# Optimization experiments

Measured on AMD Instinct MI355X. Metric: run time of the kernel, lower is better.

Reference implementation:

```python
import jax, jax.numpy as jnp
import numpy as np

N, F, E, G, NNZ = 16000, 128, 256000, 512, 512000


def _hconv(xin, row, col, hw_passed, W, b, n_nodes, n_edges):
    """PyG HypergraphConv (use_attention=False), faithful to the repo's call.
    xin: [n_nodes, Fin]; row=hyper_edge[0] (graph-edge ids), col=hyper_edge[1] (hyperedge ids).
    hw_passed: [NNZ] -- the repo passes node_weight[hyper_edge[1]]; PyG then indexes it
    again by hyperedge_index[1], so the effective per-incidence weight is hw_passed[col].
    """
    xw = xin @ W                                   # lin(x), bias=False in PyG
    w = hw_passed[col]                             # [NNZ]
    D = jax.ops.segment_sum(w, row, num_segments=n_nodes)
    Dinv = jnp.where(D == 0, 0.0, 1.0 / jnp.where(D == 0, 1.0, D))
    Bdeg = jax.ops.segment_sum(jnp.ones(row.shape, xw.dtype), col, num_segments=n_edges)
    Binv = jnp.where(Bdeg == 0, 0.0, 1.0 / jnp.where(Bdeg == 0, 1.0, Bdeg))
    # node -> hyperedge: message = B[col] * xw[row], sum over col
    out_e = jax.ops.segment_sum(Binv[col][:, None] * xw[row], col, num_segments=n_edges)
    # hyperedge -> node: message = D[row] * out_e[col], sum over row
    out = jax.ops.segment_sum(Dinv[row][:, None] * out_e[col], row, num_segments=n_nodes)
    return out + b


def setup_inputs() -> dict:
    key = jax.random.key(0)
    ks = jax.random.split(key, 20)
    rn = lambda k, shape, s=0.05: jax.random.normal(k, shape, dtype=jnp.float32) * s
    return {
        "x": jax.random.normal(ks[0], (N, F), dtype=jnp.float32),
        "graph_emb": jax.random.normal(ks[1], (G, F), dtype=jnp.float32),
        "edge_index": jax.random.randint(ks[2], (2, E), 0, N),
        "edge_type": jax.random.randint(ks[3], (E,), 0, 8),
        "batch": jnp.sort(jax.random.randint(ks[4], (N,), 0, G)),
        "hyper_edge": jnp.concatenate([
            jax.random.randint(ks[5], (1, NNZ), 0, E),   # graph-edge ids
            jax.random.randint(ks[6], (1, NNZ), 0, N)],  # hyperedge ids
            axis=0),
        # HyperWeight.lin: 2F -> F -> 1
        "hw_w1": rn(ks[7], (2 * F, F)), "hw_b1": jnp.zeros((F,), jnp.float32),
        "hw_w2": rn(ks[8], (F, 1)), "hw_b2": jnp.zeros((1,), jnp.float32),
        # HypergraphConv 1: 2F -> 2F; 2: 2F -> F (lin bias=False, separate out bias)
        "c1_w": rn(ks[9], (2 * F, 2 * F)), "c1_b": jnp.zeros((2 * F,), jnp.float32),
        "c2_w": rn(ks[10], (2 * F, F)), "c2_b": jnp.zeros((F,), jnp.float32),
        # Generator.lin: 3F -> 4F -> F
        "g_w1": rn(ks[11], (3 * F, 4 * F)), "g_b1": jnp.zeros((4 * F,), jnp.float32),
        "g_w2": rn(ks[12], (4 * F, F)), "g_b2": jnp.zeros((F,), jnp.float32),
        # classifier: 2F -> F -> 1
        "cl_w1": rn(ks[13], (2 * F, F)), "cl_b1": jnp.zeros((F,), jnp.float32),
        "cl_w2": rn(ks[14], (F, 1)), "cl_b2": jnp.zeros((1,), jnp.float32),
        "attn": jnp.array([0.5, 0.5], jnp.float32),
    }


def reference(x, graph_emb, edge_index, edge_type, batch, hyper_edge,
              hw_w1, hw_b1, hw_w2, hw_b2, c1_w, c1_b, c2_w, c2_b,
              g_w1, g_b1, g_w2, g_b2, cl_w1, cl_b1, cl_w2, cl_b2, attn):
    col, row = edge_index[0], edge_index[1]
    xij0 = jnp.concatenate([x[col], x[row]], axis=-1)          # [E, 2F]
    gemb = graph_emb[batch[edge_index[0]]]                     # [E, F] (unbatch_gemb)
    proto = graph_emb[batch]                                   # [N, F]
    # HyperWeight: per-node scalar weight
    h = jax.nn.relu(jnp.concatenate([x, proto], axis=-1) @ hw_w1 + hw_b1)
    node_w = jax.nn.sigmoid(h @ hw_w2 + hw_b2)[:, 0]           # [N]
    hrow, hcol = hyper_edge[0], hyper_edge[1]
    hw_passed = node_w[hcol]                                   # [NNZ], as in repo
    er = jax.nn.sigmoid(_hconv(xij0, hrow, hcol, hw_passed, c1_w, c1_b, E, N))
    sij = jax.nn.sigmoid(_hconv(er, hrow, hcol, hw_passed, c2_w, c2_b, E, N))  # [E, F]
    # Generator.lin on [xij, gemb]
    xl = jax.nn.relu(jnp.concatenate([xij0, gemb], axis=-1) @ g_w1 + g_b1)
    xl = jax.nn.relu(xl @ g_w2 + g_b2)                         # [E, F]
    s = attn[0] * xl + attn[1] * sij
    s = jnp.concatenate([s, gemb], axis=-1)                    # [E, 2F]
    s = jax.nn.relu(s @ cl_w1 + cl_b1)
    sij_out = jax.nn.sigmoid(s @ cl_w2 + cl_b2)                # [E, 1] (eval mode)
    return sij_out
```

## Files before the change

### kernel.cpp

```cpp
#include <hip/hip_runtime.h>
#include <hip/hip_bf16.h>

#define NODES  16000
#define FDIM   128
#define EDGES  256000
#define NNZ_   512000

typedef __attribute__((ext_vector_type(8))) short bf16x8;
typedef __attribute__((ext_vector_type(4))) float f32x4;

__device__ __forceinline__ float sigmoidf_(float z) { return 1.f / (1.f + __expf(-z)); }
__device__ __forceinline__ float bflo(unsigned u) { return __uint_as_float(u << 16); }
__device__ __forceinline__ float bfhi(unsigned u) { return __uint_as_float(u & 0xffff0000u); }
__device__ __forceinline__ unsigned pack2(float lo, float hi) {
    __hip_bfloat162 h;
    h.x = __float2bfloat16(lo);
    h.y = __float2bfloat16(hi);
    return *(unsigned*)&h;
}

__global__ __launch_bounds__(128) void hyperweight_k(
    const float* __restrict__ x, const float* __restrict__ ge, const int* __restrict__ batch,
    const float* __restrict__ w1, const float* __restrict__ b1,
    const float* __restrict__ w2, const float* __restrict__ b2, float* __restrict__ node_w)
{
    __shared__ float a[8][256];
    __shared__ float red[128];
    const int t = threadIdx.x;
    const int nb = blockIdx.x * 8;
    for (int u = 0; u < 8; ++u) {
        int n = nb + u;
        a[u][t]       = x[(size_t)n * FDIM + t];
        a[u][128 + t] = ge[(size_t)batch[n] * FDIM + t];
    }
    __syncthreads();
    float acc[8] = {0,0,0,0,0,0,0,0};
    for (int k = 0; k < 256; ++k) {
        float wv = w1[k * 128 + t];
        #pragma unroll
        for (int u = 0; u < 8; ++u) acc[u] += a[u][k] * wv;
    }
    const float wv2 = w2[t];
    for (int u = 0; u < 8; ++u) {
        float h = fmaxf(acc[u] + b1[t], 0.f);
        red[t] = h * wv2;
        __syncthreads();
        for (int s2 = 64; s2 > 0; s2 >>= 1) {
            if (t < s2) red[t] += red[t + s2];
            __syncthreads();
        }
        if (t == 0) node_w[nb + u] = sigmoidf_(red[0] + b2[0]);
        __syncthreads();
    }
}

__global__ void incidence_pass(const int* __restrict__ he, const float* __restrict__ node_w,
                               float* __restrict__ D, int* __restrict__ Bcnt, int* __restrict__ rowCnt)
{
    int i = blockIdx.x * 256 + threadIdx.x;
    if (i >= NNZ_) return;
    int hr = he[i];
    int hc = he[NNZ_ + i];
    int hc2 = he[NNZ_ + hc];
    atomicAdd(&D[hr], node_w[hc2]);
    atomicAdd(&Bcnt[hc], 1);
    atomicAdd(&rowCnt[hr], 1);
}

__global__ void inv_k(float* __restrict__ D, const int* __restrict__ Bcnt, float* __restrict__ Binv) {
    int i = blockIdx.x * 256 + threadIdx.x;
    if (i < EDGES) {
        float d = D[i];
        D[i] = (d != 0.f) ? 1.f / d : 0.f;
    }
    if (i < NODES) {
        int c = Bcnt[i];
        Binv[i] = c ? 1.f / (float)c : 0.f;
    }
}

__global__ __launch_bounds__(1024) void reduce_chunks(const int* __restrict__ in, int* __restrict__ part, int n) {
    __shared__ int s[1024];
    int t = threadIdx.x, g = blockIdx.x * 1024 + t;
    s[t] = (g < n) ? in[g] : 0;
    __syncthreads();
    for (int d = 512; d > 0; d >>= 1) {
        if (t < d) s[t] += s[t + d];
        __syncthreads();
    }
    if (t == 0) part[blockIdx.x] = s[0];
}
__global__ __launch_bounds__(1024) void scan_sums(int* __restrict__ part, int nc) {
    __shared__ int s[1024];
    int t = threadIdx.x;
    int v = (t < nc) ? part[t] : 0;
    s[t] = v;
    __syncthreads();
    for (int d = 1; d < 1024; d <<= 1) {
        int tv = (t >= d) ? s[t - d] : 0;
        __syncthreads();
        s[t] += tv;
        __syncthreads();
    }
    if (t < nc) part[t] = s[t] - v;
}
__global__ __launch_bounds__(1024) void scan_chunks(const int* __restrict__ in, const int* __restrict__ part,
                                                    int* __restrict__ out, int n) {
    __shared__ int s[1024];
    int t = threadIdx.x, g = blockIdx.x * 1024 + t;
    int v = (g < n) ? in[g] : 0;
    s[t] = v;
    __syncthreads();
    for (int d = 1; d < 1024; d <<= 1) {
        int tv = (t >= d) ? s[t - d] : 0;
        __syncthreads();
        s[t] += tv;
        __syncthreads();
    }
    int excl = s[t] - v + part[blockIdx.x];
    if (g < n) out[g] = excl;
    if (g == n - 1) out[n] = excl + v;
}

__global__ void scatter_pass(const int* __restrict__ he, const int* __restrict__ colOff, const int* __restrict__ rowOff,
                             int* __restrict__ colCur, int* __restrict__ rowCur,
                             int* __restrict__ colList, int* __restrict__ rowList)
{
    int i = blockIdx.x * 256 + threadIdx.x;
    if (i >= NNZ_) return;
    int hr = he[i];
    int hc = he[NNZ_ + i];
    int p = colOff[hc] + atomicAdd(&colCur[hc], 1);
    colList[p] = hr;
    int q = rowOff[hr] + atomicAdd(&rowCur[hr], 1);
    rowList[q] = hc;
}

__global__ void conv_bf16(const float* __restrict__ in, __hip_bfloat16* __restrict__ out, int n) {
    int i = blockIdx.x * 256 + threadIdx.x;
    if (i < n) out[i] = __float2bfloat16(in[i]);
}
__global__ void transpose_bf16(const float* __restrict__ in, __hip_bfloat16* __restrict__ out, int K, int N) {
    int i = blockIdx.x * 256 + threadIdx.x;
    if (i >= K * N) return;
    int n = i / K, k = i - n * K;
    out[i] = __float2bfloat16(in[k * N + n]);
}

__global__ __launch_bounds__(128) void col_gather_x(
    const __hip_bfloat16* __restrict__ xb, const int* __restrict__ ei,
    const int* __restrict__ colOff, const int* __restrict__ colList, float* __restrict__ agg)
{
    int n = blockIdx.x;
    int t = threadIdx.x;
    int base = (t < 64) ? 0 : EDGES;
    int f = t & 63;
    const unsigned* x32 = (const unsigned*)xb;
    int s = colOff[n], e = colOff[n + 1];
    float vx = 0.f, vy = 0.f;
    int j = s;
    for (; j + 3 < e; j += 4) {
        int r0 = colList[j], r1 = colList[j + 1], r2 = colList[j + 2], r3 = colList[j + 3];
        unsigned q0 = x32[(size_t)ei[base + r0] * 64 + f];
        unsigned q1 = x32[(size_t)ei[base + r1] * 64 + f];
        unsigned q2 = x32[(size_t)ei[base + r2] * 64 + f];
        unsigned q3 = x32[(size_t)ei[base + r3] * 64 + f];
        vx += bflo(q0) + bflo(q1) + bflo(q2) + bflo(q3);
        vy += bfhi(q0) + bfhi(q1) + bfhi(q2) + bfhi(q3);
    }
    for (; j < e; ++j) {
        unsigned q0 = x32[(size_t)ei[base + colList[j]] * 64 + f];
        vx += bflo(q0); vy += bfhi(q0);
    }
    int ob = (t < 64) ? 0 : 128;
    float2 o = make_float2(vx, vy);
    *(float2*)(agg + (size_t)n * 256 + ob + 2 * f) = o;
}

__global__ __launch_bounds__(128) void er_k(
    const __hip_bfloat16* __restrict__ oe1, const int* __restrict__ rowOff,
    const int* __restrict__ rowList, const float* __restrict__ Dinv,
    const float* __restrict__ c1b, __hip_bfloat16* __restrict__ er)
{
    int r = blockIdx.x;
    int t = threadIdx.x;
    int s = rowOff[r], e = rowOff[r + 1];
    const unsigned* o32 = (const unsigned*)oe1;
    float vx = 0.f, vy = 0.f;
    int j = s;
    for (; j + 1 < e; j += 2) {
        unsigned q0 = o32[(size_t)rowList[j] * 128 + t];
        unsigned q1 = o32[(size_t)rowList[j + 1] * 128 + t];
        vx += bflo(q0) + bflo(q1);
        vy += bfhi(q0) + bfhi(q1);
    }
    if (j < e) {
        unsigned q0 = o32[(size_t)rowList[j] * 128 + t];
        vx += bflo(q0); vy += bfhi(q0);
    }
    float dv = Dinv[r];
    *(unsigned*)(er + (size_t)r * 256 + 2 * t) =
        pack2(sigmoidf_(dv * vx + c1b[2 * t]), sigmoidf_(dv * vy + c1b[2 * t + 1]));
}

__global__ __launch_bounds__(128) void col_agg_er(
    const __hip_bfloat16* __restrict__ er, const int* __restrict__ colOff,
    const int* __restrict__ colList, float* __restrict__ agg)
{
    int n = blockIdx.x;
    int t = threadIdx.x;
    const unsigned* e32 = (const unsigned*)er;
    int s = colOff[n], e = colOff[n + 1];
    float vx = 0.f, vy = 0.f;
    int j = s;
    for (; j + 3 < e; j += 4) {
        unsigned q0 = e32[(size_t)colList[j]     * 128 + t];
        unsigned q1 = e32[(size_t)colList[j + 1] * 128 + t];
        unsigned q2 = e32[(size_t)colList[j + 2] * 128 + t];
        unsigned q3 = e32[(size_t)colList[j + 3] * 128 + t];
        vx += bflo(q0) + bflo(q1) + bflo(q2) + bflo(q3);
        vy += bfhi(q0) + bfhi(q1) + bfhi(q2) + bfhi(q3);
    }
    for (; j < e; ++j) {
        unsigned q0 = e32[(size_t)colList[j] * 128 + t];
        vx += bflo(q0); vy += bfhi(q0);
    }
    float2 o = make_float2(vx, vy);
    *(float2*)(agg + (size_t)n * 256 + 2 * t) = o;
}

template<int K, int NN, bool OB16>
__global__ __launch_bounds__(256) void gemm_node(
    const float* __restrict__ A, const float* __restrict__ B,
    const float* __restrict__ rowscale, void* __restrict__ C)
{
    __shared__ float As[16][68];
    __shared__ float Bs[16][68];
    const int tid = threadIdx.x;
    const int m0 = blockIdx.x * 64, n0 = blockIdx.y * 64;
    const int la_k = tid & 15, la_m = tid >> 4;
    const int lb_n = tid & 63, lb_k = tid >> 6;
    const int tn = tid & 15, tm = tid >> 4;
    float acc[4][4] = {};
    for (int k0 = 0; k0 < K; k0 += 16) {
        #pragma unroll
        for (int r = 0; r < 4; ++r)
            As[la_k][la_m + 16 * r] = A[(size_t)(m0 + la_m + 16 * r) * K + k0 + la_k];
        #pragma unroll
        for (int r = 0; r < 4; ++r)
            Bs[lb_k + 4 * r][lb_n] = B[(size_t)(k0 + lb_k + 4 * r) * NN + n0 + lb_n];
        __syncthreads();
        #pragma unroll
        for (int kk = 0; kk < 16; ++kk) {
            float4 av = *(const float4*)&As[kk][tm * 4];
            float4 bv = *(const float4*)&Bs[kk][tn * 4];
            float am[4] = {av.x, av.y, av.z, av.w};
            float bn[4] = {bv.x, bv.y, bv.z, bv.w};
            #pragma unroll
            for (int i = 0; i < 4; ++i)
                #pragma unroll
                for (int j = 0; j < 4; ++j)
                    acc[i][j] += am[i] * bn[j];
        }
        __syncthreads();
    }
    #pragma unroll
    for (int i = 0; i < 4; ++i) {
        int m = m0 + tm * 4 + i;
        float rs = rowscale[m];
        if constexpr (OB16) {
            __hip_bfloat16* Cp = (__hip_bfloat16*)C + (size_t)m * NN + n0 + tn * 4;
            #pragma unroll
            for (int j = 0; j < 4; ++j) Cp[j] = __float2bfloat16(rs * acc[i][j]);
        } else {
            float4 o = make_float4(rs * acc[i][0], rs * acc[i][1], rs * acc[i][2], rs * acc[i][3]);
            *(float4*)((float*)C + (size_t)m * NN + n0 + tn * 4) = o;
        }
    }
}

template<int K, int LDB>
__global__ __launch_bounds__(256) void xw_mfma(
    const __hip_bfloat16* __restrict__ A, const __hip_bfloat16* __restrict__ Bt,
    __hip_bfloat16* __restrict__ dst)
{
    __shared__ __align__(16) __hip_bfloat16 As[64][40];
    __shared__ __align__(16) __hip_bfloat16 Bs[128][40];
    const int tid = threadIdx.x;
    const int m0 = blockIdx.x * 64, n0 = blockIdx.y * 128;
    const int wave = tid >> 6, lane = tid & 63;
    const int wr = wave >> 1, wc = wave & 1;
    const int srow = tid >> 2, kseg = (tid & 3) * 8;
    const int nr = tid >> 1, kb = (tid & 1) * 16;
    const int fr = lane & 15, krow = (lane >> 4) * 8, rq = lane >> 4;

    f32x4 acc[2][4] = {};
    for (int k0 = 0; k0 < K; k0 += 32) {
        *(uint4*)&As[srow][kseg] = *(const uint4*)(A + (size_t)(m0 + srow) * K + k0 + kseg);
        *(uint4*)&Bs[nr][kb]     = *(const uint4*)(Bt + (size_t)(n0 + nr) * LDB + k0 + kb);
        *(uint4*)&Bs[nr][kb + 8] = *(const uint4*)(Bt + (size_t)(n0 + nr) * LDB + k0 + kb + 8);
        __syncthreads();
        bf16x8 af[2], bf[4];
        #pragma unroll
        for (int i = 0; i < 2; ++i) af[i] = *(const bf16x8*)&As[wr * 32 + i * 16 + fr][krow];
        #pragma unroll
        for (int j = 0; j < 4; ++j) bf[j] = *(const bf16x8*)&Bs[wc * 64 + j * 16 + fr][krow];
        #pragma unroll
        for (int i = 0; i < 2; ++i)
            #pragma unroll
            for (int j = 0; j < 4; ++j)
                acc[i][j] = __builtin_amdgcn_mfma_f32_16x16x32_bf16(af[i], bf[j], acc[i][j], 0, 0, 0);
        __syncthreads();
    }
    #pragma unroll
    for (int i = 0; i < 2; ++i)
        #pragma unroll
        for (int j = 0; j < 4; ++j) {
            int col = n0 + wc * 64 + j * 16 + fr;
            #pragma unroll
            for (int r = 0; r < 4; ++r) {
                int row = m0 + wr * 32 + i * 16 + rq * 4 + r;
                dst[(size_t)row * 512 + col] = __float2bfloat16(acc[i][j][r]);
            }
        }
}

__global__ __launch_bounds__(256) void gen2_mfma(
    const __hip_bfloat16* __restrict__ xa, const __hip_bfloat16* __restrict__ xb2,
    const __hip_bfloat16* __restrict__ gc, const float* __restrict__ b1,
    const __hip_bfloat16* __restrict__ gw2t, const float* __restrict__ b2,
    const int* __restrict__ ei, const int* __restrict__ batch,
    __hip_bfloat16* __restrict__ xl2)
{
    __shared__ __align__(16) __hip_bfloat16 As[2][64][40];
    __shared__ __align__(16) __hip_bfloat16 Bs[2][128][40];
    const int tid = threadIdx.x;
    const int m0 = blockIdx.x * 64;
    const int wave = tid >> 6, lane = tid & 63;
    const int wr = wave >> 1, wc = wave & 1;
    const int srow = tid >> 2, kseg = (tid & 3) * 8;
    const int nr = tid >> 1, kb = (tid & 1) * 16;
    const int fr = lane & 15, krow = (lane >> 4) * 8, rq = lane >> 4;

    const int eg = m0 + srow;
    const int c = ei[eg];
    const __hip_bfloat16* pa = xa  + (size_t)c * 512;
    const __hip_bfloat16* pb = xb2 + (size_t)ei[EDGES + eg] * 512;
    const __hip_bfloat16* pc = gc  + (size_t)batch[c] * 512;

    uint4 ua, ub, uc, bv0, bv1;
    auto GLOAD = [&](int k0) {
        int kg = k0 + kseg;
        ua = *(const uint4*)(pa + kg);
        ub = *(const uint4*)(pb + kg);
        uc = *(const uint4*)(pc + kg);
        bv0 = *(const uint4*)(gw2t + (size_t)nr * 512 + k0 + kb);
        bv1 = *(const uint4*)(gw2t + (size_t)nr * 512 + k0 + kb + 8);
    };
    auto STORE = [&](int buf, int k0) {
        int kg = k0 + kseg;
        float4 f0 = *(const float4*)(b1 + kg);
        float4 f1 = *(const float4*)(b1 + kg + 4);
        uint4 av;
        av.x = pack2(fmaxf(bflo(ua.x) + bflo(ub.x) + bflo(uc.x) + f0.x, 0.f),
                     fmaxf(bfhi(ua.x) + bfhi(ub.x) + bfhi(uc.x) + f0.y, 0.f));
        av.y = pack2(fmaxf(bflo(ua.y) + bflo(ub.y) + bflo(uc.y) + f0.z, 0.f),
                     fmaxf(bfhi(ua.y) + bfhi(ub.y) + bfhi(uc.y) + f0.w, 0.f));
        av.z = pack2(fmaxf(bflo(ua.z) + bflo(ub.z) + bflo(uc.z) + f1.x, 0.f),
                     fmaxf(bfhi(ua.z) + bfhi(ub.z) + bfhi(uc.z) + f1.y, 0.f));
        av.w = pack2(fmaxf(bflo(ua.w) + bflo(ub.w) + bflo(uc.w) + f1.z, 0.f),
                     fmaxf(bfhi(ua.w) + bfhi(ub.w) + bfhi(uc.w) + f1.w, 0.f));
        *(uint4*)&As[buf][srow][kseg] = av;
        *(uint4*)&Bs[buf][nr][kb]     = bv0;
        *(uint4*)&Bs[buf][nr][kb + 8] = bv1;
    };

    GLOAD(0);
    STORE(0, 0);
    __syncthreads();

    f32x4 acc[2][4] = {};
    for (int it = 0; it < 16; ++it) {
        int cur = it & 1;
        if (it < 15) GLOAD((it + 1) * 32);
        bf16x8 af[2], bf[4];
        #pragma unroll
        for (int i = 0; i < 2; ++i) af[i] = *(const bf16x8*)&As[cur][wr * 32 + i * 16 + fr][krow];
        #pragma unroll
        for (int j = 0; j < 4; ++j) bf[j] = *(const bf16x8*)&Bs[cur][wc * 64 + j * 16 + fr][krow];
        #pragma unroll
        for (int i = 0; i < 2; ++i)
            #pragma unroll
            for (int j = 0; j < 4; ++j)
                acc[i][j] = __builtin_amdgcn_mfma_f32_16x16x32_bf16(af[i], bf[j], acc[i][j], 0, 0, 0);
        if (it < 15) STORE(cur ^ 1, (it + 1) * 32);
        __syncthreads();
    }
    #pragma unroll
    for (int i = 0; i < 2; ++i)
        #pragma unroll
        for (int j = 0; j < 4; ++j) {
            int col = wc * 64 + j * 16 + fr;
            float bc = b2[col];
            #pragma unroll
            for (int r = 0; r < 4; ++r) {
                int row = m0 + wr * 32 + i * 16 + rq * 4 + r;
                xl2[(size_t)row * 128 + col] = __float2bfloat16(fmaxf(acc[i][j][r] + bc, 0.f));
            }
        }
}

__global__ __launch_bounds__(256) void cls_mfma(
    const __hip_bfloat16* __restrict__ xl2, const __hip_bfloat16* __restrict__ oe2,
    const __hip_bfloat16* __restrict__ geb, const float* __restrict__ attn,
    const __hip_bfloat16* __restrict__ clw1t, const float* __restrict__ b1,
    const float* __restrict__ w2, const float* __restrict__ b2, const float* __restrict__ c2b,
    const int* __restrict__ ei, const int* __restrict__ batch,
    const int* __restrict__ rowOff, const int* __restrict__ rowList, const float* __restrict__ Dinv,
    float* __restrict__ out)
{
    __shared__ __align__(16) __hip_bfloat16 As[2][64][40];
    __shared__ __align__(16) __hip_bfloat16 Bs[2][128][40];
    const int tid = threadIdx.x;
    const int m0 = blockIdx.x * 64;
    const int wave = tid >> 6, lane = tid & 63;
    const int srow = tid >> 2, kseg = (tid & 3) * 8;
    const int nr = tid >> 1, kb = (tid & 1) * 16;
    const int fr = lane & 15, krow = (lane >> 4) * 8, rq = lane >> 4;

    const int eg = m0 + srow;
    const int gi = batch[ei[eg]];
    const float a0 = attn[0], a1 = attn[1];
    const int rs = rowOff[eg], re = rowOff[eg + 1];
    const float dv = Dinv[eg];

    uint4 avr, bv0, bv1;
    auto PREP = [&](int k0) {
        int kg = k0 + kseg;
        bv0 = *(const uint4*)(clw1t + (size_t)nr * 256 + k0 + kb);
        bv1 = *(const uint4*)(clw1t + (size_t)nr * 256 + k0 + kb + 8);
        if (kg < 128) {
            uint4 u = *(const uint4*)(xl2 + (size_t)eg * 128 + kg);
            float s0 = 0.f, s1 = 0.f, s2 = 0.f, s3 = 0.f, s4 = 0.f, s5 = 0.f, s6 = 0.f, s7 = 0.f;
            for (int q = rs; q < re; ++q) {
                uint4 o = *(const uint4*)(oe2 + (size_t)rowList[q] * 128 + kg);
                s0 += bflo(o.x); s1 += bfhi(o.x); s2 += bflo(o.y); s3 += bfhi(o.y);
                s4 += bflo(o.z); s5 += bfhi(o.z); s6 += bflo(o.w); s7 += bfhi(o.w);
            }
            float4 c0 = *(const float4*)(c2b + kg);
            float4 c1 = *(const float4*)(c2b + kg + 4);
            avr.x = pack2(a0 * bflo(u.x) + a1 * sigmoidf_(dv * s0 + c0.x),
                          a0 * bfhi(u.x) + a1 * sigmoidf_(dv * s1 + c0.y));
            avr.y = pack2(a0 * bflo(u.y) + a1 * sigmoidf_(dv * s2 + c0.z),
                          a0 * bfhi(u.y) + a1 * sigmoidf_(dv * s3 + c0.w));
            avr.z = pack2(a0 * bflo(u.z) + a1 * sigmoidf_(dv * s4 + c1.x),
                          a0 * bfhi(u.z) + a1 * sigmoidf_(dv * s5 + c1.y));
            avr.w = pack2(a0 * bflo(u.w) + a1 * sigmoidf_(dv * s6 + c1.z),
                          a0 * bfhi(u.w) + a1 * sigmoidf_(dv * s7 + c1.w));
        } else {
            avr = *(const uint4*)(geb + (size_t)gi * 128 + kg - 128);
        }
    };
    auto STORE = [&](int buf) {
        *(uint4*)&As[buf][srow][kseg] = avr;
        *(uint4*)&Bs[buf][nr][kb]     = bv0;
        *(uint4*)&Bs[buf][nr][kb + 8] = bv1;
    };

    PREP(0);
    STORE(0);
    __syncthreads();

    f32x4 acc[8] = {};
    for (int it = 0; it < 8; ++it) {
        int cur = it & 1;
        if (it < 7) PREP((it + 1) * 32);
        bf16x8 af = *(const bf16x8*)&As[cur][wave * 16 + fr][krow];
        #pragma unroll
        for (int j = 0; j < 8; ++j) {
            bf16x8 bf = *(const bf16x8*)&Bs[cur][j * 16 + fr][krow];
            acc[j] = __builtin_amdgcn_mfma_f32_16x16x32_bf16(af, bf, acc[j], 0, 0, 0);
        }
        if (it < 7) STORE(cur ^ 1);
        __syncthreads();
    }
    float rsum[4] = {0.f, 0.f, 0.f, 0.f};
    #pragma unroll
    for (int j = 0; j < 8; ++j) {
        int colg = j * 16 + fr;
        float bc = b1[colg];
        float wv = w2[colg];
        #pragma unroll
        for (int r = 0; r < 4; ++r)
            rsum[r] += fmaxf(acc[j][r] + bc, 0.f) * wv;
    }
    #pragma unroll
    for (int m = 1; m < 16; m <<= 1) {
        #pragma unroll
        for (int r = 0; r < 4; ++r) rsum[r] += __shfl_xor(rsum[r], m, 64);
    }
    if (fr == 0) {
        float bb = b2[0];
        #pragma unroll
        for (int r = 0; r < 4; ++r)
            out[m0 + wave * 16 + rq * 4 + r] = sigmoidf_(rsum[r] + bb);
    }
}

extern "C" void kernel_launch(void* const* d_in, const int* in_sizes, int n_in,
                              void* d_out, int out_size, void* d_ws, size_t ws_size,
                              hipStream_t stream)
{
    const float* x     = (const float*)d_in[0];
    const float* ge    = (const float*)d_in[1];
    const int*   ei    = (const int*)d_in[2];
    const int*   batch = (const int*)d_in[4];
    const int*   he    = (const int*)d_in[5];
    const float* hw_w1 = (const float*)d_in[6];
    const float* hw_b1 = (const float*)d_in[7];
    const float* hw_w2 = (const float*)d_in[8];
    const float* hw_b2 = (const float*)d_in[9];
    const float* c1_w  = (const float*)d_in[10];
    const float* c1_b  = (const float*)d_in[11];
    const float* c2_w  = (const float*)d_in[12];
    const float* c2_b  = (const float*)d_in[13];
    const float* g_w1  = (const float*)d_in[14];
    const float* g_b1  = (const float*)d_in[15];
    const float* g_w2  = (const float*)d_in[16];
    const float* g_b2  = (const float*)d_in[17];
    const float* cl_w1 = (const float*)d_in[18];
    const float* cl_b1 = (const float*)d_in[19];
    const float* cl_w2 = (const float*)d_in[20];
    const float* cl_b2 = (const float*)d_in[21];
    const float* attn  = (const float*)d_in[22];
    float* out = (float*)d_out;

    char* ws = (char*)d_ws;
    size_t off = 0;
    auto alloc = [&](size_t nb) -> void* {
        off = (off + 255) & ~(size_t)255;
        void* p = ws + off;
        off += nb;
        return p;
    };
    float* D      = (float*)alloc((size_t)EDGES * 4);
    int*   Bcnt   = (int*)  alloc((size_t)NODES * 4);
    int*   rowCnt = (int*)  alloc((size_t)EDGES * 4);
    int*   colCur = (int*)  alloc((size_t)NODES * 4);
    int*   rowCur = (int*)  alloc((size_t)EDGES * 4);
    size_t zero_end = off;
    float* node_w = (float*)alloc((size_t)NODES * 4);
    float* Binv   = (float*)alloc((size_t)NODES * 4);
    int*   colOff = (int*)  alloc((size_t)(NODES + 1) * 4);
    int*   rowOff = (int*)  alloc((size_t)(EDGES + 1) * 4);
    int*   colList= (int*)  alloc((size_t)NNZ_ * 4);
    int*   rowList= (int*)  alloc((size_t)NNZ_ * 4);
    int*   partA  = (int*)  alloc(1024 * 4);
    int*   partB  = (int*)  alloc(1024 * 4);
    __hip_bfloat16* xb    = (__hip_bfloat16*)alloc((size_t)NODES * FDIM * 2);
    __hip_bfloat16* geb   = (__hip_bfloat16*)alloc((size_t)512 * FDIM * 2);
    __hip_bfloat16* gw1t  = (__hip_bfloat16*)alloc((size_t)512 * 384 * 2);
    __hip_bfloat16* gw2t  = (__hip_bfloat16*)alloc((size_t)128 * 512 * 2);
    __hip_bfloat16* clw1t = (__hip_bfloat16*)alloc((size_t)128 * 256 * 2);
    __hip_bfloat16* xa    = (__hip_bfloat16*)alloc((size_t)NODES * 512 * 2);
    __hip_bfloat16* xb2   = (__hip_bfloat16*)alloc((size_t)NODES * 512 * 2);
    __hip_bfloat16* gc    = (__hip_bfloat16*)alloc((size_t)512 * 512 * 2);
    float* agg  = (float*)alloc((size_t)NODES * 256 * 4);
    __hip_bfloat16* oe1b = (__hip_bfloat16*)alloc((size_t)NODES * 256 * 2);
    __hip_bfloat16* oe2  = (__hip_bfloat16*)alloc((size_t)NODES * 128 * 2);
    __hip_bfloat16* er   = (__hip_bfloat16*)alloc((size_t)EDGES * 256 * 2);
    __hip_bfloat16* xl2  = er;

    hipMemsetAsync(D, 0, zero_end, stream);

    hyperweight_k<<<NODES / 8, 128, 0, stream>>>(x, ge, batch, hw_w1, hw_b1, hw_w2, hw_b2, node_w);
    incidence_pass<<<NNZ_ / 256, 256, 0, stream>>>(he, node_w, D, Bcnt, rowCnt);
    inv_k<<<EDGES / 256, 256, 0, stream>>>(D, Bcnt, Binv);

    const int ncN = (NODES + 1023) / 1024;
    const int ncE = (EDGES + 1023) / 1024;
    reduce_chunks<<<ncN, 1024, 0, stream>>>(Bcnt, partA, NODES);
    scan_sums<<<1, 1024, 0, stream>>>(partA, ncN);
    scan_chunks<<<ncN, 1024, 0, stream>>>(Bcnt, partA, colOff, NODES);
    reduce_chunks<<<ncE, 1024, 0, stream>>>(rowCnt, partB, EDGES);
    scan_sums<<<1, 1024, 0, stream>>>(partB, ncE);
    scan_chunks<<<ncE, 1024, 0, stream>>>(rowCnt, partB, rowOff, EDGES);
    scatter_pass<<<NNZ_ / 256, 256, 0, stream>>>(he, colOff, rowOff, colCur, rowCur, colList, rowList);

    conv_bf16<<<(NODES * FDIM + 255) / 256, 256, 0, stream>>>(x, xb, NODES * FDIM);
    conv_bf16<<<(512 * FDIM + 255) / 256, 256, 0, stream>>>(ge, geb, 512 * FDIM);
    transpose_bf16<<<(384 * 512 + 255) / 256, 256, 0, stream>>>(g_w1, gw1t, 384, 512);
    transpose_bf16<<<(512 * 128 + 255) / 256, 256, 0, stream>>>(g_w2, gw2t, 512, 128);
    transpose_bf16<<<(256 * 128 + 255) / 256, 256, 0, stream>>>(cl_w1, clw1t, 256, 128);

    xw_mfma<128, 384><<<dim3(NODES / 64, 4), 256, 0, stream>>>(xb, gw1t, xa);
    xw_mfma<128, 384><<<dim3(NODES / 64, 4), 256, 0, stream>>>(xb, gw1t + 128, xb2);
    xw_mfma<128, 384><<<dim3(512 / 64, 4), 256, 0, stream>>>(geb, gw1t + 256, gc);

    col_gather_x<<<NODES, 128, 0, stream>>>(xb, ei, colOff, colList, agg);
    gemm_node<256, 256, true><<<dim3(NODES / 64, 4), 256, 0, stream>>>(agg, c1_w, Binv, oe1b);

    er_k<<<EDGES, 128, 0, stream>>>(oe1b, rowOff, rowList, D, c1_b, er);
    col_agg_er<<<NODES, 128, 0, stream>>>(er, colOff, colList, agg);
    gemm_node<256, 128, true><<<dim3(NODES / 64, 2), 256, 0, stream>>>(agg, c2_w, Binv, oe2);

    gen2_mfma<<<EDGES / 64, 256, 0, stream>>>(xa, xb2, gc, g_b1, gw2t, g_b2, ei, batch, xl2);

    cls_mfma<<<EDGES / 64, 256, 0, stream>>>(xl2, oe2, geb, attn, clw1t, cl_b1, cl_w2, cl_b2,
                                             c2_b, ei, batch, rowOff, rowList, D, out);
}
```

Baseline: 770.5 us.

## Fuse generator and classifier edge GEMMs, fold graph term into xa, switch to fp16

Merges gen2_mfma and cls_mfma into one kernel that keeps the 64x128 generator output tile in shared memory, so the per-edge intermediate never goes through global memory. The graph-embedding projection and first bias are added into the per-node xa product at its epilogue, which removes one gather and add per edge in the hot loop. Edge-side operands move to fp16 so the add and relu can use packed v_pk_add/v_pk_max. In exchange the fused kernel drops the software double-buffering, uses more LDS per block, and fp16 has less range than bf16.

New measurement: 731.1 us. -5.1%, faster.

```diff
diff --git a/kernel.cpp b/kernel.cpp
--- a/kernel.cpp
+++ b/kernel.cpp
@@ -1,5 +1,6 @@
 #include <hip/hip_runtime.h>
 #include <hip/hip_bf16.h>
+#include <hip/hip_fp16.h>
 
 #define NODES  16000
 #define FDIM   128
@@ -7,6 +8,7 @@
 #define NNZ_   512000
 
 typedef __attribute__((ext_vector_type(8))) short bf16x8;
+typedef __attribute__((ext_vector_type(8))) _Float16 f16x8;
 typedef __attribute__((ext_vector_type(4))) float f32x4;
 
 __device__ __forceinline__ float sigmoidf_(float z) { return 1.f / (1.f + __expf(-z)); }
@@ -17,6 +19,19 @@
     h.x = __float2bfloat16(lo);
     h.y = __float2bfloat16(hi);
     return *(unsigned*)&h;
+}
+__device__ __forceinline__ unsigned pk_add_f16(unsigned a, unsigned b) {
+    unsigned r; asm("v_pk_add_f16 %0, %1, %2" : "=v"(r) : "v"(a), "v"(b)); return r;
+}
+__device__ __forceinline__ unsigned pk_relu_f16(unsigned a) {
+    unsigned r; asm("v_pk_max_f16 %0, %1, %2" : "=v"(r) : "v"(a), "v"(0u)); return r;
+}
+__device__ __forceinline__ unsigned pkh(float lo, float hi) {
+    __half2 h = __floats2half2_rn(lo, hi);
+    return *(unsigned*)&h;
+}
+__device__ __forceinline__ float2 h2f2(unsigned u) {
+    return __half22float2(*(__half2*)&u);
 }
 
 __global__ __launch_bounds__(128) void hyperweight_k(
@@ -136,15 +151,20 @@
     rowList[q] = hc;
 }
 
-__global__ void conv_bf16(const float* __restrict__ in, __hip_bfloat16* __restrict__ out, int n) {
+__global__ void conv_x(const float* __restrict__ in, __hip_bfloat16* __restrict__ ob,
+                       _Float16* __restrict__ oh, int n) {
     int i = blockIdx.x * 256 + threadIdx.x;
-    if (i < n) out[i] = __float2bfloat16(in[i]);
-}
-__global__ void transpose_bf16(const float* __restrict__ in, __hip_bfloat16* __restrict__ out, int K, int N) {
+    if (i < n) { float v = in[i]; ob[i] = __float2bfloat16(v); oh[i] = (_Float16)v; }
+}
+__global__ void conv_f16(const float* __restrict__ in, _Float16* __restrict__ out, int n) {
+    int i = blockIdx.x * 256 + threadIdx.x;
+    if (i < n) out[i] = (_Float16)in[i];
+}
+__global__ void transpose_f16(const float* __restrict__ in, _Float16* __restrict__ out, int K, int N) {
     int i = blockIdx.x * 256 + threadIdx.x;
     if (i >= K * N) return;
     int n = i / K, k = i - n * K;
-    out[i] = __float2bfloat16(in[k * N + n]);
+    out[i] = (_Float16)in[k * N + n];
 }
 
 __global__ __launch_bounds__(128) void col_gather_x(
@@ -279,13 +299,13 @@
     }
 }
 
-template<int K, int LDB>
-__global__ __launch_bounds__(256) void xw_mfma(
-    const __hip_bfloat16* __restrict__ A, const __hip_bfloat16* __restrict__ Bt,
-    __hip_bfloat16* __restrict__ dst)
-{
-    __shared__ __align__(16) __hip_bfloat16 As[64][40];
-    __shared__ __align__(16) __hip_bfloat16 Bs[128][40];
+template<int LDB, bool XAG>
+__global__ __launch_bounds__(256) void xw_f16(
+    const _Float16* __restrict__ A, const _Float16* __restrict__ Bt, _Float16* __restrict__ dst,
+    const _Float16* __restrict__ gct, const int* __restrict__ batch, const float* __restrict__ bias)
+{
+    __shared__ __align__(16) _Float16 As[64][40];
+    __shared__ __align__(16) _Float16 Bs[128][40];
     const int tid = threadIdx.x;
     const int m0 = blockIdx.x * 64, n0 = blockIdx.y * 128;
     const int wave = tid >> 6, lane = tid & 63;
@@ -295,21 +315,21 @@
     const int fr = lane & 15, krow = (lane >> 4) * 8, rq = lane >> 4;
 
     f32x4 acc[2][4] = {};
-    for (int k0 = 0; k0 < K; k0 += 32) {
-        *(uint4*)&As[srow][kseg] = *(const uint4*)(A + (size_t)(m0 + srow) * K + k0 + kseg);
+    for (int k0 = 0; k0 < 128; k0 += 32) {
+        *(uint4*)&As[srow][kseg] = *(const uint4*)(A + (size_t)(m0 + srow) * 128 + k0 + kseg);
         *(uint4*)&Bs[nr][kb]     = *(const uint4*)(Bt + (size_t)(n0 + nr) * LDB + k0 + kb);
         *(uint4*)&Bs[nr][kb + 8] = *(const uint4*)(Bt + (size_t)(n0 + nr) * LDB + k0 + kb + 8);
         __syncthreads();
-        bf16x8 af[2], bf[4];
-        #pragma unroll
-        for (int i = 0; i < 2; ++i) af[i] = *(const bf16x8*)&As[wr * 32 + i * 16 + fr][krow];
-        #pragma unroll
-        for (int j = 0; j < 4; ++j) bf[j] = *(const bf16x8*)&Bs[wc * 64 + j * 16 + fr][krow];
+        f16x8 af[2], bf[4];
+        #pragma unroll
+        for (int i = 0; i < 2; ++i) af[i] = *(const f16x8*)&As[wr * 32 + i * 16 + fr][krow];
+        #pragma unroll
+        for (int j = 0; j < 4; ++j) bf[j] = *(const f16x8*)&Bs[wc * 64 + j * 16 + fr][krow];
         #pragma unroll
         for (int i = 0; i < 2; ++i)
             #pragma unroll
             for (int j = 0; j < 4; ++j)
-                acc[i][j] = __builtin_amdgcn_mfma_f32_16x16x32_bf16(af[i], bf[j], acc[i][j], 0, 0, 0);
+                acc[i][j] = __builtin_amdgcn_mfma_f32_16x16x32_f16(af[i], bf[j], acc[i][j], 0, 0, 0);
         __syncthreads();
     }
     #pragma unroll
@@ -320,20 +340,28 @@
             #pragma unroll
             for (int r = 0; r < 4; ++r) {
                 int row = m0 + wr * 32 + i * 16 + rq * 4 + r;
-                dst[(size_t)row * 512 + col] = __float2bfloat16(acc[i][j][r]);
+                float v = acc[i][j][r];
+                if constexpr (XAG)
+                    v += (float)gct[(size_t)batch[row] * 512 + col] + bias[col];
+                dst[(size_t)row * 512 + col] = (_Float16)v;
             }
         }
 }
 
-__global__ __launch_bounds__(256) void gen2_mfma(
-    const __hip_bfloat16* __restrict__ xa, const __hip_bfloat16* __restrict__ xb2,
-    const __hip_bfloat16* __restrict__ gc, const float* __restrict__ b1,
-    const __hip_bfloat16* __restrict__ gw2t, const float* __restrict__ b2,
+__global__ __launch_bounds__(256) void gencls_mfma(
+    const _Float16* __restrict__ xag, const _Float16* __restrict__ xb2,
+    const _Float16* __restrict__ gw2t, const float* __restrict__ gb2,
+    const _Float16* __restrict__ geh, const float* __restrict__ attn,
+    const _Float16* __restrict__ clw1t, const float* __restrict__ clb1,
+    const float* __restrict__ w2, const float* __restrict__ b2, const float* __restrict__ c2b,
+    const __hip_bfloat16* __restrict__ oe2,
     const int* __restrict__ ei, const int* __restrict__ batch,
-    __hip_bfloat16* __restrict__ xl2)
-{
-    __shared__ __align__(16) __hip_bfloat16 As[2][64][40];
-    __shared__ __align__(16) __hip_bfloat16 Bs[2][128][40];
+    const int* __restrict__ rowOff, const int* __restrict__ rowList, const float* __restrict__ Dinv,
+    float* __restrict__ out)
+{
+    __shared__ __align__(16) _Float16 As[64][40];
+    __shared__ __align__(16) _Float16 Bs[128][40];
+    __shared__ __align__(16) _Float16 xlt[64][128];
     const int tid = threadIdx.x;
     const int m0 = blockIdx.x * 64;
     const int wave = tid >> 6, lane = tid & 63;
@@ -343,57 +371,37 @@
     const int fr = lane & 15, krow = (lane >> 4) * 8, rq = lane >> 4;
 
     const int eg = m0 + srow;
-    const int c = ei[eg];
-    const __hip_bfloat16* pa = xa  + (size_t)c * 512;
-    const __hip_bfloat16* pb = xb2 + (size_t)ei[EDGES + eg] * 512;
-    const __hip_bfloat16* pc = gc  + (size_t)batch[c] * 512;
-
-    uint4 ua, ub, uc, bv0, bv1;
-    auto GLOAD = [&](int k0) {
+    const int cnode = ei[eg];
+    const _Float16* pa = xag + (size_t)cnode * 512;
+    const _Float16* pb = xb2 + (size_t)ei[EDGES + eg] * 512;
+    const int gi = batch[cnode];
+    const int rs = rowOff[eg], re = rowOff[eg + 1];
+    const float dv = Dinv[eg];
+
+    f32x4 acc[2][4] = {};
+    for (int k0 = 0; k0 < 512; k0 += 32) {
         int kg = k0 + kseg;
-        ua = *(const uint4*)(pa + kg);
-        ub = *(const uint4*)(pb + kg);
-        uc = *(const uint4*)(pc + kg);
-        bv0 = *(const uint4*)(gw2t + (size_t)nr * 512 + k0 + kb);
-        bv1 = *(const uint4*)(gw2t + (size_t)nr * 512 + k0 + kb + 8);
-    };
-    auto STORE = [&](int buf, int k0) {
-        int kg = k0 + kseg;
-        float4 f0 = *(const float4*)(b1 + kg);
-        float4 f1 = *(const float4*)(b1 + kg + 4);
+        uint4 ua = *(const uint4*)(pa + kg);
+        uint4 ub = *(const uint4*)(pb + kg);
         uint4 av;
-        av.x = pack2(fmaxf(bflo(ua.x) + bflo(ub.x) + bflo(uc.x) + f0.x, 0.f),
-                     fmaxf(bfhi(ua.x) + bfhi(ub.x) + bfhi(uc.x) + f0.y, 0.f));
-        av.y = pack2(fmaxf(bflo(ua.y) + bflo(ub.y) + bflo(uc.y) + f0.z, 0.f),
-                     fmaxf(bfhi(ua.y) + bfhi(ub.y) + bfhi(uc.y) + f0.w, 0.f));
-        av.z = pack2(fmaxf(bflo(ua.z) + bflo(ub.z) + bflo(uc.z) + f1.x, 0.f),
-                     fmaxf(bfhi(ua.z) + bfhi(ub.z) + bfhi(uc.z) + f1.y, 0.f));
-        av.w = pack2(fmaxf(bflo(ua.w) + bflo(ub.w) + bflo(uc.w) + f1.z, 0.f),
-                     fmaxf(bfhi(ua.w) + bfhi(ub.w) + bfhi(uc.w) + f1.w, 0.f));
-        *(uint4*)&As[buf][srow][kseg] = av;
-        *(uint4*)&Bs[buf][nr][kb]     = bv0;
-        *(uint4*)&Bs[buf][nr][kb + 8] = bv1;
-    };
-
-    GLOAD(0);
-    STORE(0, 0);
-    __syncthreads();
-
-    f32x4 acc[2][4] = {};
-    for (int it = 0; it < 16; ++it) {
-        int cur = it & 1;
-        if (it < 15) GLOAD((it + 1) * 32);
-        bf16x8 af[2], bf[4];
-        #pragma unroll
-        for (int i = 0; i < 2; ++i) af[i] = *(const bf16x8*)&As[cur][wr * 32 + i * 16 + fr][krow];
-        #pragma unroll
-        for (int j = 0; j < 4; ++j) bf[j] = *(const bf16x8*)&Bs[cur][wc * 64 + j * 16 + fr][krow];
+        av.x = pk_relu_f16(pk_add_f16(ua.x, ub.x));
+        av.y = pk_relu_f16(pk_add_f16(ua.y, ub.y));
+        av.z = pk_relu_f16(pk_add_f16(ua.z, ub.z));
+        av.w = pk_relu_f16(pk_add_f16(ua.w, ub.w));
+        *(uint4*)&As[srow][kseg] = av;
+        *(uint4*)&Bs[nr][kb]     = *(const uint4*)(gw2t + (size_t)nr * 512 + k0 + kb);
+        *(uint4*)&Bs[nr][kb + 8] = *(const uint4*)(gw2t + (size_t)nr * 512 + k0 + kb + 8);
+        __syncthreads();
+        f16x8 af[2], bf[4];
+        #pragma unroll
+        for (int i = 0; i < 2; ++i) af[i] = *(const f16x8*)&As[wr * 32 + i * 16 + fr][krow];
+        #pragma unroll
+        for (int j = 0; j < 4; ++j) bf[j] = *(const f16x8*)&Bs[wc * 64 + j * 16 + fr][krow];
         #pragma unroll
         for (int i = 0; i < 2; ++i)
             #pragma unroll
             for (int j = 0; j < 4; ++j)
-                acc[i][j] = __builtin_amdgcn_mfma_f32_16x16x32_bf16(af[i], bf[j], acc[i][j], 0, 0, 0);
-        if (it < 15) STORE(cur ^ 1, (it + 1) * 32);
+                acc[i][j] = __builtin_amdgcn_mfma_f32_16x16x32_f16(af[i], bf[j], acc[i][j], 0, 0, 0);
         __syncthreads();
     }
     #pragma unroll
@@ -401,46 +409,22 @@
         #pragma unroll
         for (int j = 0; j < 4; ++j) {
             int col = wc * 64 + j * 16 + fr;
-            float bc = b2[col];
+            float bc = gb2[col];
             #pragma unroll
             for (int r = 0; r < 4; ++r) {
-                int row = m0 + wr * 32 + i * 16 + rq * 4 + r;
-                xl2[(size_t)row * 128 + col] = __float2bfloat16(fmaxf(acc[i][j][r] + bc, 0.f));
+                int row = wr * 32 + i * 16 + rq * 4 + r;
+                xlt[row][col] = (_Float16)fmaxf(acc[i][j][r] + bc, 0.f);
             }
         }
-}
-
-__global__ __launch_bounds__(256) void cls_mfma(
-    const __hip_bfloat16* __restrict__ xl2, const __hip_bfloat16* __restrict__ oe2,
-    const __hip_bfloat16* __restrict__ geb, const float* __restrict__ attn,
-    const __hip_bfloat16* __restrict__ clw1t, const float* __restrict__ b1,
-    const float* __restrict__ w2, const float* __restrict__ b2, const float* __restrict__ c2b,
-    const int* __restrict__ ei, const int* __restrict__ batch,
-    const int* __restrict__ rowOff, const int* __restrict__ rowList, const float* __restrict__ Dinv,
-    float* __restrict__ out)
-{
-    __shared__ __align__(16) __hip_bfloat16 As[2][64][40];
-    __shared__ __align__(16) __hip_bfloat16 Bs[2][128][40];
-    const int tid = threadIdx.x;
-    const int m0 = blockIdx.x * 64;
-    const int wave = tid >> 6, lane = tid & 63;
-    const int srow = tid >> 2, kseg = (tid & 3) * 8;
-    const int nr = tid >> 1, kb = (tid & 1) * 16;
-    const int fr = lane & 15, krow = (lane >> 4) * 8, rq = lane >> 4;
-
-    const int eg = m0 + srow;
-    const int gi = batch[ei[eg]];
+    __syncthreads();
+
     const float a0 = attn[0], a1 = attn[1];
-    const int rs = rowOff[eg], re = rowOff[eg + 1];
-    const float dv = Dinv[eg];
-
-    uint4 avr, bv0, bv1;
-    auto PREP = [&](int k0) {
-        int kg = k0 + kseg;
-        bv0 = *(const uint4*)(clw1t + (size_t)nr * 256 + k0 + kb);
-        bv1 = *(const uint4*)(clw1t + (size_t)nr * 256 + k0 + kb + 8);
+    f32x4 acc2[8] = {};
+    for (int it = 0; it < 8; ++it) {
+        int k0 = it * 32, kg = k0 + kseg;
+        uint4 av;
         if (kg < 128) {
-            uint4 u = *(const uint4*)(xl2 + (size_t)eg * 128 + kg);
+            uint4 u = *(const uint4*)&xlt[srow][kg];
             float s0 = 0.f, s1 = 0.f, s2 = 0.f, s3 = 0.f, s4 = 0.f, s5 = 0.f, s6 = 0.f, s7 = 0.f;
             for (int q = rs; q < re; ++q) {
                 uint4 o = *(const uint4*)(oe2 + (size_t)rowList[q] * 128 + kg);
@@ -449,50 +433,39 @@
             }
             float4 c0 = *(const float4*)(c2b + kg);
             float4 c1 = *(const float4*)(c2b + kg + 4);
-            avr.x = pack2(a0 * bflo(u.x) + a1 * sigmoidf_(dv * s0 + c0.x),
-                          a0 * bfhi(u.x) + a1 * sigmoidf_(dv * s1 + c0.y));
-            avr.y = pack2(a0 * bflo(u.y) + a1 * sigmoidf_(dv * s2 + c0.z),
-                          a0 * bfhi(u.y) + a1 * sigmoidf_(dv * s3 + c0.w));
-            avr.z = pack2(a0 * bflo(u.z) + a1 * sigmoidf_(dv * s4 + c1.x),
-                          a0 * bfhi(u.z) + a1 * sigmoidf_(dv * s5 + c1.y));
-            avr.w = pack2(a0 * bflo(u.w) + a1 * sigmoidf_(dv * s6 + c1.z),
-                          a0 * bfhi(u.w) + a1 * sigmoidf_(dv * s7 + c1.w));
+            float2 f0 = h2f2(u.x), f1 = h2f2(u.y), f2 = h2f2(u.z), f3 = h2f2(u.w);
+            av.x = pkh(a0 * f0.x + a1 * sigmoidf_(dv * s0 + c0.x),
+                       a0 * f0.y + a1 * sigmoidf_(dv * s1 + c0.y));
+            av.y = pkh(a0 * f1.x + a1 * sigmoidf_(dv * s2 + c0.z),
+                       a0 * f1.y + a1 * sigmoidf_(dv * s3 + c0.w));
+            av.z = pkh(a0 * f2.x + a1 * sigmoidf_(dv * s4 + c1.x),
+                       a0 * f2.y + a1 * sigmoidf_(dv * s5 + c1.y));
+            av.w = pkh(a0 * f3.x + a1 * sigmoidf_(dv * s6 + c1.z),
+                       a0 * f3.y + a1 * sigmoidf_(dv * s7 + c1.w));
         } else {
-            avr = *(const uint4*)(geb + (size_t)gi * 128 + kg - 128);
-        }
-    };
-    auto STORE = [&](int buf) {
-        *(uint4*)&As[buf][srow][kseg] = avr;
-        *(uint4*)&Bs[buf][nr][kb]     = bv0;
-        *(uint4*)&Bs[buf][nr][kb + 8] = bv1;
-    };
-
-    PREP(0);
-    STORE(0);
-    __syncthreads();
-
-    f32x4 acc[8] = {};
-    for (int it = 0; it < 8; ++it) {
-        int cur = it & 1;
-        if (it < 7) PREP((it + 1) * 32);
-        bf16x8 af = *(const bf16x8*)&As[cur][wave * 16 + fr][krow];
+            av = *(const uint4*)(geh + (size_t)gi * 128 + kg - 128);
+        }
+        *(uint4*)&As[srow][kseg] = av;
+        *(uint4*)&Bs[nr][kb]     = *(const uint4*)(clw1t + (size_t)nr * 256 + k0 + kb);
+        *(uint4*)&Bs[nr][kb + 8] = *(const uint4*)(clw1t + (size_t)nr * 256 + k0 + kb + 8);
+        __syncthreads();
+        f16x8 af = *(const f16x8*)&As[wave * 16 + fr][krow];
         #pragma unroll
         for (int j = 0; j < 8; ++j) {
-            bf16x8 bf = *(const bf16x8*)&Bs[cur][j * 16 + fr][krow];
-            acc[j] = __builtin_amdgcn_mfma_f32_16x16x32_bf16(af, bf, acc[j], 0, 0, 0);
-        }
-        if (it < 7) STORE(cur ^ 1);
+            f16x8 bf = *(const f16x8*)&Bs[j * 16 + fr][krow];
+            acc2[j] = __builtin_amdgcn_mfma_f32_16x16x32_f16(af, bf, acc2[j], 0, 0, 0);
+        }
         __syncthreads();
     }
     float rsum[4] = {0.f, 0.f, 0.f, 0.f};
     #pragma unroll
     for (int j = 0; j < 8; ++j) {
         int colg = j * 16 + fr;
-        float bc = b1[colg];
+        float bc = clb1[colg];
         float wv = w2[colg];
         #pragma unroll
         for (int r = 0; r < 4; ++r)
-            rsum[r] += fmaxf(acc[j][r] + bc, 0.f) * wv;
+            rsum[r] += fmaxf(acc2[j][r] + bc, 0.f) * wv;
     }
     #pragma unroll
     for (int m = 1; m < 16; m <<= 1) {
@@ -558,18 +531,18 @@
     int*   partA  = (int*)  alloc(1024 * 4);
     int*   partB  = (int*)  alloc(1024 * 4);
     __hip_bfloat16* xb    = (__hip_bfloat16*)alloc((size_t)NODES * FDIM * 2);
-    __hip_bfloat16* geb   = (__hip_bfloat16*)alloc((size_t)512 * FDIM * 2);
-    __hip_bfloat16* gw1t  = (__hip_bfloat16*)alloc((size_t)512 * 384 * 2);
-    __hip_bfloat16* gw2t  = (__hip_bfloat16*)alloc((size_t)128 * 512 * 2);
-    __hip_bfloat16* clw1t = (__hip_bfloat16*)alloc((size_t)128 * 256 * 2);
-    __hip_bfloat16* xa    = (__hip_bfloat16*)alloc((size_t)NODES * 512 * 2);
-    __hip_bfloat16* xb2   = (__hip_bfloat16*)alloc((size_t)NODES * 512 * 2);
-    __hip_bfloat16* gc    = (__hip_bfloat16*)alloc((size_t)512 * 512 * 2);
+    _Float16* xh    = (_Float16*)alloc((size_t)NODES * FDIM * 2);
+    _Float16* geh   = (_Float16*)alloc((size_t)512 * FDIM * 2);
+    _Float16* gw1t  = (_Float16*)alloc((size_t)512 * 384 * 2);
+    _Float16* gw2t  = (_Float16*)alloc((size_t)128 * 512 * 2);
+    _Float16* clw1t = (_Float16*)alloc((size_t)128 * 256 * 2);
+    _Float16* xag   = (_Float16*)alloc((size_t)NODES * 512 * 2);
+    _Float16* xb2   = (_Float16*)alloc((size_t)NODES * 512 * 2);
+    _Float16* gc    = (_Float16*)alloc((size_t)512 * 512 * 2);
     float* agg  = (float*)alloc((size_t)NODES * 256 * 4);
     __hip_bfloat16* oe1b = (__hip_bfloat16*)alloc((size_t)NODES * 256 * 2);
     __hip_bfloat16* oe2  = (__hip_bfloat16*)alloc((size_t)NODES * 128 * 2);
     __hip_bfloat16* er   = (__hip_bfloat16*)alloc((size_t)EDGES * 256 * 2);
-    __hip_bfloat16* xl2  = er;
 
     hipMemsetAsync(D, 0, zero_end, stream);
 
@@ -587,15 +560,15 @@
     scan_chunks<<<ncE, 1024, 0, stream>>>(rowCnt, partB, rowOff, EDGES);
     scatter_pass<<<NNZ_ / 256, 256, 0, stream>>>(he, colOff, rowOff, colCur, rowCur, colList, rowList);
 
-    conv_bf16<<<(NODES * FDIM + 255) / 256, 256, 0, stream>>>(x, xb, NODES * FDIM);
-    conv_bf16<<<(512 * FDIM + 255) / 256, 256, 0, stream>>>(ge, geb, 512 * FDIM);
-    transpose_bf16<<<(384 * 512 + 255) / 256, 256, 0, stream>>>(g_w1, gw1t, 384, 512);
-    transpose_bf16<<<(512 * 128 + 255) / 256, 256, 0, stream>>>(g_w2, gw2t, 512, 128);
-    transpose_bf16<<<(256 * 128 + 255) / 256, 256, 0, stream>>>(cl_w1, clw1t, 256, 128);
-
-    xw_mfma<128, 384><<<dim3(NODES / 64, 4), 256, 0, stream>>>(xb, gw1t, xa);
-    xw_mfma<128, 384><<<dim3(NODES / 64, 4), 256, 0, stream>>>(xb, gw1t + 128, xb2);
-    xw_mfma<128, 384><<<dim3(512 / 64, 4), 256, 0, stream>>>(geb, gw1t + 256, gc);
+    conv_x<<<(NODES * FDIM + 255) / 256, 256, 0, stream>>>(x, xb, xh, NODES * FDIM);
+    conv_f16<<<(512 * FDIM + 255) / 256, 256, 0, stream>>>(ge, geh, 512 * FDIM);
+    transpose_f16<<<(384 * 512 + 255) / 256, 256, 0, stream>>>(g_w1, gw1t, 384, 512);
+    transpose_f16<<<(512 * 128 + 255) / 256, 256, 0, stream>>>(g_w2, gw2t, 512, 128);
+    transpose_f16<<<(256 * 128 + 255) / 256, 256, 0, stream>>>(cl_w1, clw1t, 256, 128);
+
+    xw_f16<384, false><<<dim3(512 / 64, 4), 256, 0, stream>>>(geh, gw1t + 256, gc, nullptr, nullptr, nullptr);
+    xw_f16<384, true><<<dim3(NODES / 64, 4), 256, 0, stream>>>(xh, gw1t, xag, gc, batch, g_b1);
+    xw_f16<384, false><<<dim3(NODES / 64, 4), 256, 0, stream>>>(xh, gw1t + 128, xb2, nullptr, nullptr, nullptr);
 
     col_gather_x<<<NODES, 128, 0, stream>>>(xb, ei, colOff, colList, agg);
     gemm_node<256, 256, true><<<dim3(NODES / 64, 4), 256, 0, stream>>>(agg, c1_w, Binv, oe1b);
@@ -604,8 +577,7 @@
     col_agg_er<<<NODES, 128, 0, stream>>>(er, colOff, colList, agg);
     gemm_node<256, 128, true><<<dim3(NODES / 64, 2), 256, 0, stream>>>(agg, c2_w, Binv, oe2);
 
-    gen2_mfma<<<EDGES / 64, 256, 0, stream>>>(xa, xb2, gc, g_b1, gw2t, g_b2, ei, batch, xl2);
-
-    cls_mfma<<<EDGES / 64, 256, 0, stream>>>(xl2, oe2, geb, attn, clw1t, cl_b1, cl_w2, cl_b2,
-                                             c2_b, ei, batch, rowOff, rowList, D, out);
-}
+    gencls_mfma<<<EDGES / 64, 256, 0, stream>>>(xag, xb2, gw2t, g_b2, geh, attn, clw1t, cl_b1,
+                                                cl_w2, cl_b2, c2_b, oe2, ei, batch,
+                                                rowOff, rowList, D, out);
+}
```
